# Kernel tuning notes

Measured on AMD Instinct MI355X. Metric: run time of the kernel, lower is better.

The kernel has to match this reference:

```python
import jax, jax.numpy as jnp
import numpy as np

B, C_IN, IMG, PATCH = 16, 3, 512, 16
C_FEAT, N_CLS, K = 2048, 18, 24  # K cells per image (fixed -> jit-friendly ragged groups)
HF = IMG // PATCH  # 32
N_CELLS = B * K
EPS = 1e-6


def setup_inputs() -> dict:
    key = jax.random.key(0)
    ks = jax.random.split(key, 8)
    return {
        "cell_img": jax.random.normal(ks[0], (B, C_IN, IMG, IMG), jnp.float32),
        "cell_masks": jax.random.uniform(ks[1], (N_CELLS, HF, HF), jnp.float32),
        "cell_counts": jnp.full((B,), K, dtype=jnp.int32),
        "W_backbone": jax.random.normal(ks[2], (C_FEAT, C_IN, PATCH, PATCH), jnp.float32) * 0.02,
        "b_backbone": jnp.zeros((C_FEAT,), jnp.float32),
        "W_final": jax.random.normal(ks[3], (N_CLS, C_FEAT, 1, 1), jnp.float32) * 0.02,
        "b_final": jnp.zeros((N_CLS,), jnp.float32),
        "W1": jax.random.normal(ks[4], (1024, C_FEAT), jnp.float32) * 0.02,
        "b1": jnp.zeros((1024,), jnp.float32),
        "W2": jax.random.normal(ks[5], (N_CLS, 1024), jnp.float32) * 0.02,
        "b2": jnp.zeros((N_CLS,), jnp.float32),
    }


def _forward(cell_img, cell_masks, cell_counts, W_backbone, b_backbone,
             W_final, b_final, W1, b1, W2, b2):
    # backbone: patch-embed style conv, 3 -> 2048, stride 16 -> [B, 2048, 32, 32]
    fm = jax.lax.conv_general_dilated(
        cell_img, W_backbone, (PATCH, PATCH), "VALID",
        dimension_numbers=("NCHW", "OIHW", "NCHW"))
    fm = jax.nn.relu(fm + b_backbone[None, :, None, None])
    # final_conv: 1x1 conv 2048 -> 18 class maps
    class_maps = jnp.einsum("bchw,oc->bohw", fm, W_final[:, :, 0, 0]) + b_final[None, :, None, None]

    # masked-RoI average pooling (feature_roi / class_roi)
    fm2 = fm.reshape(B, C_FEAT, HF * HF)            # [B, C, P]
    cm2 = class_maps.reshape(B, N_CLS, HF * HF)     # [B, 18, P]
    masksB = cell_masks.reshape(B, K, HF * HF)      # [B, K, P]
    area = masksB.sum(-1, keepdims=True) + EPS       # [B, K, 1]
    cell_features = jnp.einsum("bkp,bcp->bkc", masksB, fm2) / area   # [B, K, 2048]
    cell_class_logits = jnp.einsum("bkp,bcp->bkc", masksB, cm2) / area  # [B, K, 18]

    # fc_cell_weights (Dropout is identity at eval)
    h = jax.nn.relu(jnp.einsum("bkc,oc->bko", cell_features, W1) + b1)
    cell_weight_logits = jnp.einsum("bkh,oh->bko", h, W2) + b2       # [B, K, 18]

    # per-image (segment) softmax over cells + attention-weighted sum
    attn = jax.nn.softmax(cell_weight_logits, axis=1)
    logits = (attn * cell_class_logits).sum(axis=1)                  # [B, 18]

    # zero-count fallback: global max-pool of class maps
    fallback = class_maps.max(axis=(2, 3))
    return jnp.where((cell_counts > 0)[:, None], logits, fallback)


def reference(cell_img, cell_masks, cell_counts, W_backbone, b_backbone,
              W_final, b_final, W1, b1, W2, b2):
    return _forward(cell_img, cell_masks, cell_counts, W_backbone, b_backbone,
                    W_final, b_final, W1, b1, W2, b2)
```

## Files before the change

### kernel.cpp

```cpp
#include <hip/hip_runtime.h>
#include <hip/hip_bf16.h>

#define B_      16
#define C_IN    3
#define IMG     512
#define PATCH   16
#define C_FEAT  2048
#define N_CLS   18
#define KCELL   24
#define HF      32
#define P_      (HF*HF)
#define KDIM    (C_IN*PATCH*PATCH)
#define M_GEMM1 (B_*P_)
#define EPS_    1e-6f

typedef __attribute__((ext_vector_type(8))) short bf16x8;
typedef __attribute__((ext_vector_type(4))) float f32x4;
typedef __attribute__((ext_vector_type(4))) unsigned short us4;
typedef __attribute__((ext_vector_type(8))) unsigned short us8;
typedef __attribute__((ext_vector_type(4))) float fl4;

#define DEVFN static __device__ __forceinline__

DEVFN unsigned short f2bf(float f) {
  union { float f; unsigned u; } x; x.f = f;
  unsigned r = (x.u + 0x7fffu + ((x.u >> 16) & 1u)) >> 16;
  return (unsigned short)r;
}
DEVFN unsigned short f2bf_h(float f) {
  __hip_bfloat16 h = __float2bfloat16(f);
  return *reinterpret_cast<unsigned short*>(&h);
}
DEVFN float bf2f(unsigned short u) {
  union { unsigned u; float f; } x; x.u = ((unsigned)u) << 16;
  return x.f;
}
DEVFN f32x4 mfma16(bf16x8 a, bf16x8 b, f32x4 c) {
  return __builtin_amdgcn_mfma_f32_16x16x32_bf16(a, b, c, 0, 0, 0);
}
#define GLOAD16(gp, lp) __builtin_amdgcn_global_load_lds( \
    (const __attribute__((address_space(1))) unsigned int*)(gp), \
    (__attribute__((address_space(3))) unsigned int*)(lp), 16, 0, 0)

#define OFF_A     0u
#define OFF_WB    25165824u
#define OFF_W1    28311552u
#define OFF_W2    32505856u
#define OFF_FM    32542720u
#define OFF_MB    99651584u
#define OFF_AREA  100700160u
#define OFF_CF    100702208u
#define OFF_CL    102275072u
#define OFF_H     102302720u
#define WS_NEED   103089152u

__global__ __launch_bounds__(256) void k_prep(const float* __restrict__ masks,
                                              const float* __restrict__ Wb,
                                              const float* __restrict__ W1,
                                              const float* __restrict__ W2,
                                              unsigned short* __restrict__ mb,
                                              float* __restrict__ area,
                                              unsigned short* __restrict__ Wbb,
                                              unsigned short* __restrict__ W1b,
                                              unsigned short* __restrict__ W2b) {
  int blk = blockIdx.x;
  int t = threadIdx.x;
  if (blk < 512) {
    int b = blk >> 5, m = blk & 31;
    unsigned short* dst = mb + ((size_t)(b * 32 + m)) * P_;
    float s = 0.f;
    if (m < KCELL) {
      const float* src = masks + ((size_t)(b * KCELL + m)) * P_;
      for (int p = t; p < P_; p += 256) { float v = src[p]; s += v; dst[p] = f2bf(v); }
    } else {
      for (int p = t; p < P_; p += 256) dst[p] = 0;
    }
    for (int off = 32; off; off >>= 1) s += __shfl_down(s, off);
    __shared__ float red[4];
    if ((t & 63) == 0) red[t >> 6] = s;
    __syncthreads();
    if (t == 0) area[b * 32 + m] = red[0] + red[1] + red[2] + red[3] + EPS_;
    return;
  }
  const float* src; unsigned short* dst; int local, n;
  if (blk < 1280)      { src = Wb; dst = Wbb; local = blk - 512;  n = C_FEAT * KDIM; }
  else if (blk < 2304) { src = W1; dst = W1b; local = blk - 1280; n = 1024 * C_FEAT; }
  else                 { src = W2; dst = W2b; local = blk - 2304; n = N_CLS * 1024; }
  int i = (local * 256 + t) * 8;
  if (i + 8 <= n) {
    fl4 v0 = *(const fl4*)(src + i);
    fl4 v1 = *(const fl4*)(src + i + 4);
    us8 o;
    o[0] = f2bf(v0[0]); o[1] = f2bf(v0[1]); o[2] = f2bf(v0[2]); o[3] = f2bf(v0[3]);
    o[4] = f2bf(v1[0]); o[5] = f2bf(v1[1]); o[6] = f2bf(v1[2]); o[7] = f2bf(v1[3]);
    *(us8*)(dst + i) = o;
  }
}

__global__ __launch_bounds__(256) void k_gemm1f(const float* __restrict__ img,
                                                const unsigned short* __restrict__ BT,
                                                const float* __restrict__ bias,
                                                unsigned short* __restrict__ CT) {
  __shared__ float          As[8 * 1024];
  __shared__ unsigned short Bs[4 * 2048];
  int bid = blockIdx.x;
  int swz = (bid & 7) * 256 + (bid >> 3);
  int bm = swz >> 4, bn = swz & 15;
  int m0 = bm * 128, n0 = bn * 128;
  int t = threadIdx.x;
  int w = t >> 6, l = t & 63, lr = l & 15, lg = l >> 4;
  int wr = w >> 1, wc = w & 1;

  int arow = t >> 1;
  int am = m0 + arow;
  int ab = am >> 10, ap = am & 1023, ahf = ap >> 5, awf = ap & 31;
  const float* imb = img + ((size_t)(ab * 3) * 512 + (size_t)ahf * 16) * 512 + awf * 16;
  int kq = (t & 1) * 4;

  f32x4 acc[4][4] = {};
  for (int k0 = 0; k0 < KDIM; k0 += 64) {
#pragma unroll
    for (int j = 0; j < 8; ++j) {
      int k = k0 + j * 8 + kq;
      int c = k >> 8, py = (k >> 4) & 15, px = k & 15;
      GLOAD16(imb + ((size_t)c * 512 + py) * 512 + px, As + j * 1024 + t * 4);
    }
#pragma unroll
    for (int g = 0; g < 4; ++g)
      GLOAD16(BT + (size_t)(n0 + (t >> 1)) * KDIM + k0 + g * 16 + (t & 1) * 8,
              Bs + g * 2048 + t * 8);
    __syncthreads();
#pragma unroll
    for (int kk = 0; kk < 64; kk += 32) {
      bf16x8 a[4], bb[4];
#pragma unroll
      for (int mi = 0; mi < 4; ++mi) {
        int row = wr * 64 + mi * 16 + lr;
        int o = (kk >> 3) + lg;
        const float* ap_ = As + o * 1024 + row * 8;
        fl4 lo = *(const fl4*)ap_;
        fl4 hi = *(const fl4*)(ap_ + 4);
        us8 af;
        af[0] = f2bf_h(lo[0]); af[1] = f2bf_h(lo[1]); af[2] = f2bf_h(lo[2]); af[3] = f2bf_h(lo[3]);
        af[4] = f2bf_h(hi[0]); af[5] = f2bf_h(hi[1]); af[6] = f2bf_h(hi[2]); af[7] = f2bf_h(hi[3]);
        a[mi] = *(bf16x8*)&af;
      }
#pragma unroll
      for (int ni = 0; ni < 4; ++ni) {
        int row = wc * 64 + ni * 16 + lr;
        int g = (kk >> 4) + (lg >> 1), half = lg & 1;
        bb[ni] = *(const bf16x8*)(Bs + g * 2048 + row * 16 + half * 8);
      }
#pragma unroll
      for (int mi = 0; mi < 4; ++mi)
#pragma unroll
        for (int ni = 0; ni < 4; ++ni)
          acc[mi][ni] = mfma16(a[mi], bb[ni], acc[mi][ni]);
    }
    __syncthreads();
  }
  int b = m0 >> 10;
  int pbase0 = (m0 & 1023) + wr * 64 + lg * 4;
#pragma unroll
  for (int ni = 0; ni < 4; ++ni) {
    int gcol = n0 + wc * 64 + ni * 16 + lr;
    float bv = bias[gcol];
    unsigned short* crow = CT + ((size_t)(b * C_FEAT + gcol)) * P_;
#pragma unroll
    for (int mi = 0; mi < 4; ++mi) {
      us4 o;
#pragma unroll
      for (int r = 0; r < 4; ++r)
        o[r] = f2bf(fmaxf(acc[mi][ni][r] + bv, 0.f));
      *(us4*)(crow + pbase0 + mi * 16) = o;
    }
  }
}

__global__ __launch_bounds__(256) void k_pool(const unsigned short* __restrict__ mb,
                                              const unsigned short* __restrict__ fmT,
                                              const float* __restrict__ area,
                                              unsigned short* __restrict__ CF) {
  int b = blockIdx.x, ct = blockIdx.y;
  int t = threadIdx.x, w = t >> 6, l = t & 63, lr = l & 15, lg = l >> 4;
  int c0 = ct * 128 + w * 32;
  const unsigned short* mbb = mb + (size_t)b * 32 * P_;
  const unsigned short* fb = fmT + (size_t)b * C_FEAT * P_;
  f32x4 acc[2][2] = {};
#pragma unroll 2
  for (int k0 = 0; k0 < P_; k0 += 32) {
    int kb = k0 + lg * 8;
    bf16x8 a0 = *(const bf16x8*)(mbb + (size_t)lr * P_ + kb);
    bf16x8 a1 = *(const bf16x8*)(mbb + (size_t)(16 + lr) * P_ + kb);
    bf16x8 b0 = *(const bf16x8*)(fb + (size_t)(c0 + lr) * P_ + kb);
    bf16x8 b1 = *(const bf16x8*)(fb + (size_t)(c0 + 16 + lr) * P_ + kb);
    acc[0][0] = mfma16(a0, b0, acc[0][0]);
    acc[1][0] = mfma16(a1, b0, acc[1][0]);
    acc[0][1] = mfma16(a0, b1, acc[0][1]);
    acc[1][1] = mfma16(a1, b1, acc[1][1]);
  }
#pragma unroll
  for (int mt = 0; mt < 2; ++mt)
#pragma unroll
    for (int r = 0; r < 4; ++r) {
      int m = mt * 16 + lg * 4 + r;
      if (m < KCELL) {
        float inv = 1.f / area[b * 32 + m];
#pragma unroll
        for (int nt = 0; nt < 2; ++nt) {
          int c = c0 + nt * 16 + lr;
          CF[((size_t)(b * KCELL + m)) * C_FEAT + c] = f2bf(acc[mt][nt][r] * inv);
        }
      }
    }
}

__global__ __launch_bounds__(256) void k_class_logits(const unsigned short* __restrict__ CF,
                                                      const float* __restrict__ Wf,
                                                      const float* __restrict__ bfin,
                                                      const float* __restrict__ area,
                                                      float* __restrict__ cl) {
  int cell = blockIdx.x;
  int t = threadIdx.x;
  int c0 = t * 8;
  float cf[8];
  bf16x8 v = *(const bf16x8*)(CF + (size_t)cell * C_FEAT + c0);
#pragma unroll
  for (int j = 0; j < 8; ++j) cf[j] = bf2f((unsigned short)v[j]);
  float acc[N_CLS];
#pragma unroll
  for (int o = 0; o < N_CLS; ++o) {
    fl4 w0 = *(const fl4*)(Wf + (size_t)o * C_FEAT + c0);
    fl4 w1 = *(const fl4*)(Wf + (size_t)o * C_FEAT + c0 + 4);
    acc[o] = cf[0]*w0[0] + cf[1]*w0[1] + cf[2]*w0[2] + cf[3]*w0[3]
           + cf[4]*w1[0] + cf[5]*w1[1] + cf[6]*w1[2] + cf[7]*w1[3];
  }
#pragma unroll
  for (int o = 0; o < N_CLS; ++o)
    for (int off = 32; off; off >>= 1) acc[o] += __shfl_down(acc[o], off);
  __shared__ float red[4][N_CLS];
  if ((t & 63) == 0) {
#pragma unroll
    for (int o = 0; o < N_CLS; ++o) red[t >> 6][o] = acc[o];
  }
  __syncthreads();
  if (t < N_CLS) {
    int b = cell / KCELL, m = cell % KCELL;
    float ar = area[b * 32 + m];
    float coeff = (ar - EPS_) / ar;
    cl[(size_t)cell * N_CLS + t] =
        red[0][t] + red[1][t] + red[2][t] + red[3][t] + bfin[t] * coeff;
  }
}

__global__ __launch_bounds__(256) void k_mlp1(const unsigned short* __restrict__ CF,
                                              const unsigned short* __restrict__ W1b,
                                              const float* __restrict__ b1,
                                              unsigned short* __restrict__ h) {
  int wid = blockIdx.x * 4 + (threadIdx.x >> 6);
  int l = threadIdx.x & 63, lr = l & 15, lg = l >> 4;
  int mt = wid >> 6, nt = wid & 63;
  int m0 = mt * 16, n0 = nt * 16;
  f32x4 acc = {};
  for (int k0 = 0; k0 < C_FEAT; k0 += 32) {
    int kb = k0 + lg * 8;
    bf16x8 a = *(const bf16x8*)(CF + (size_t)(m0 + lr) * C_FEAT + kb);
    bf16x8 b = *(const bf16x8*)(W1b + (size_t)(n0 + lr) * C_FEAT + kb);
    acc = mfma16(a, b, acc);
  }
  int col = n0 + lr;
  float bv = b1[col];
#pragma unroll
  for (int r = 0; r < 4; ++r) {
    int row = m0 + lg * 4 + r;
    h[(size_t)row * 1024 + col] = f2bf(fmaxf(acc[r] + bv, 0.f));
  }
}

__global__ __launch_bounds__(512) void k_mlp2_final(const unsigned short* __restrict__ hbf,
                                                    const unsigned short* __restrict__ W2b,
                                                    const float* __restrict__ b2,
                                                    const float* __restrict__ cl,
                                                    float* __restrict__ out) {
  int b = blockIdx.x;
  int t = threadIdx.x;
  __shared__ float wl[KCELL][N_CLS + 2];
  if (t < KCELL * N_CLS) {
    int k = t / N_CLS, o = t % N_CLS;
    const unsigned short* hr = hbf + (size_t)(b * KCELL + k) * 1024;
    const unsigned short* wr = W2b + (size_t)o * 1024;
    float acc = 0.f;
    for (int c = 0; c < 1024; c += 16) {
      bf16x8 hv0 = *(const bf16x8*)(hr + c);
      bf16x8 hv1 = *(const bf16x8*)(hr + c + 8);
      bf16x8 wv0 = *(const bf16x8*)(wr + c);
      bf16x8 wv1 = *(const bf16x8*)(wr + c + 8);
#pragma unroll
      for (int j = 0; j < 8; ++j)
        acc += bf2f((unsigned short)hv0[j]) * bf2f((unsigned short)wv0[j])
             + bf2f((unsigned short)hv1[j]) * bf2f((unsigned short)wv1[j]);
    }
    wl[k][o] = acc + b2[o];
  }
  __syncthreads();
  if (t < N_CLS) {
    float m = -3.4e38f;
    for (int k = 0; k < KCELL; ++k) m = fmaxf(m, wl[k][t]);
    float s = 0.f, num = 0.f;
    for (int k = 0; k < KCELL; ++k) {
      float e = expf(wl[k][t] - m);
      s += e;
      num += e * cl[(size_t)(b * KCELL + k) * N_CLS + t];
    }
    out[b * N_CLS + t] = num / s;
  }
}

__global__ __launch_bounds__(256) void k_fallback(const int* __restrict__ counts,
                                                  const unsigned short* __restrict__ fmT,
                                                  const float* __restrict__ Wf,
                                                  const float* __restrict__ bfin,
                                                  float* __restrict__ out) {
  int b = blockIdx.x;
  if (counts[b] > 0) return;
  int t = threadIdx.x;
  const unsigned short* fb = fmT + (size_t)b * C_FEAT * P_;
  float lmax[N_CLS];
#pragma unroll
  for (int o = 0; o < N_CLS; ++o) lmax[o] = -3.4e38f;
  for (int p = t; p < P_; p += 256) {
    float acc[N_CLS];
#pragma unroll
    for (int o = 0; o < N_CLS; ++o) acc[o] = bfin[o];
    for (int c = 0; c < C_FEAT; ++c) {
      float f = bf2f(fb[(size_t)c * P_ + p]);
#pragma unroll
      for (int o = 0; o < N_CLS; ++o) acc[o] += f * Wf[(size_t)o * C_FEAT + c];
    }
#pragma unroll
    for (int o = 0; o < N_CLS; ++o) lmax[o] = fmaxf(lmax[o], acc[o]);
  }
#pragma unroll
  for (int o = 0; o < N_CLS; ++o)
    for (int off = 32; off; off >>= 1) lmax[o] = fmaxf(lmax[o], __shfl_down(lmax[o], off));
  __shared__ float red[4][N_CLS];
  if ((t & 63) == 0) {
#pragma unroll
    for (int o = 0; o < N_CLS; ++o) red[t >> 6][o] = lmax[o];
  }
  __syncthreads();
  if (t < N_CLS)
    out[b * N_CLS + t] = fmaxf(fmaxf(red[0][t], red[1][t]), fmaxf(red[2][t], red[3][t]));
}

extern "C" void kernel_launch(void* const* d_in, const int* in_sizes, int n_in,
                              void* d_out, int out_size, void* d_ws, size_t ws_size,
                              hipStream_t stream) {
  const float* img    = (const float*)d_in[0];
  const float* masks  = (const float*)d_in[1];
  const int*   counts = (const int*)d_in[2];
  const float* Wb     = (const float*)d_in[3];
  const float* bb     = (const float*)d_in[4];
  const float* Wf     = (const float*)d_in[5];
  const float* bfin   = (const float*)d_in[6];
  const float* W1     = (const float*)d_in[7];
  const float* b1     = (const float*)d_in[8];
  const float* W2     = (const float*)d_in[9];
  const float* b2     = (const float*)d_in[10];
  float* out = (float*)d_out;

  char* ws = (char*)d_ws;
  unsigned short* Wbb  = (unsigned short*)(ws + OFF_WB);
  unsigned short* W1b  = (unsigned short*)(ws + OFF_W1);
  unsigned short* W2b  = (unsigned short*)(ws + OFF_W2);
  unsigned short* fmT  = (unsigned short*)(ws + OFF_FM);
  unsigned short* mbb  = (unsigned short*)(ws + OFF_MB);
  float*          area = (float*)(ws + OFF_AREA);
  unsigned short* CF   = (unsigned short*)(ws + OFF_CF);
  float*          cl   = (float*)(ws + OFF_CL);
  unsigned short* hb   = (unsigned short*)(ws + OFF_H);

  k_prep<<<2313, 256, 0, stream>>>(masks, Wb, W1, W2, mbb, area, Wbb, W1b, W2b);
  k_gemm1f<<<(M_GEMM1 / 128) * (C_FEAT / 128), 256, 0, stream>>>(img, Wbb, bb, fmT);
  k_pool<<<dim3(B_, C_FEAT / 128), 256, 0, stream>>>(mbb, fmT, area, CF);
  k_class_logits<<<B_ * KCELL, 256, 0, stream>>>(CF, Wf, bfin, area, cl);
  k_mlp1<<<(24 * 64) / 4, 256, 0, stream>>>(CF, W1b, b1, hb);
  k_mlp2_final<<<B_, 512, 0, stream>>>(hb, W2b, b2, cl, out);
  k_fallback<<<B_, 256, 0, stream>>>(counts, fmT, Wf, bfin, out);
}
```

Baseline: 280.7 us.

## Fuse masked RoI pooling into backbone GEMM epilogue, drop feature-map round trip

The backbone GEMM now keeps its 128x128 output tile in LDS and multiplies it right away by the masks for that spatial slice. It writes per-slice fp32 partial cell features, so the full bf16 feature map (~64MB) never goes to global memory. A new post kernel sums the 8 slice partials, computes mask areas and class logits, and replaces the separate prep, pool and class-logit kernels. Image tiles are converted to bf16 once on load into a swizzled LDS layout rather than at every fragment read. W1/W2 are converted in the MLP kernels instead of a prep pass. The fallback now recomputes the backbone directly from the image, which is very slow but runs only when a count is zero.

Result: slower. 334.4 us (+19.1%).

```diff
diff --git a/kernel.cpp b/kernel.cpp
--- a/kernel.cpp
+++ b/kernel.cpp
@@ -42,67 +42,30 @@
     (const __attribute__((address_space(1))) unsigned int*)(gp), \
     (__attribute__((address_space(3))) unsigned int*)(lp), 16, 0, 0)
 
-#define OFF_A     0u
+#define OFF_CFP   0u
 #define OFF_WB    25165824u
-#define OFF_W1    28311552u
-#define OFF_W2    32505856u
-#define OFF_FM    32542720u
-#define OFF_MB    99651584u
-#define OFF_AREA  100700160u
 #define OFF_CF    100702208u
 #define OFF_CL    102275072u
 #define OFF_H     102302720u
-#define WS_NEED   103089152u
-
-__global__ __launch_bounds__(256) void k_prep(const float* __restrict__ masks,
-                                              const float* __restrict__ Wb,
-                                              const float* __restrict__ W1,
-                                              const float* __restrict__ W2,
-                                              unsigned short* __restrict__ mb,
-                                              float* __restrict__ area,
-                                              unsigned short* __restrict__ Wbb,
-                                              unsigned short* __restrict__ W1b,
-                                              unsigned short* __restrict__ W2b) {
-  int blk = blockIdx.x;
-  int t = threadIdx.x;
-  if (blk < 512) {
-    int b = blk >> 5, m = blk & 31;
-    unsigned short* dst = mb + ((size_t)(b * 32 + m)) * P_;
-    float s = 0.f;
-    if (m < KCELL) {
-      const float* src = masks + ((size_t)(b * KCELL + m)) * P_;
-      for (int p = t; p < P_; p += 256) { float v = src[p]; s += v; dst[p] = f2bf(v); }
-    } else {
-      for (int p = t; p < P_; p += 256) dst[p] = 0;
-    }
-    for (int off = 32; off; off >>= 1) s += __shfl_down(s, off);
-    __shared__ float red[4];
-    if ((t & 63) == 0) red[t >> 6] = s;
-    __syncthreads();
-    if (t == 0) area[b * 32 + m] = red[0] + red[1] + red[2] + red[3] + EPS_;
-    return;
-  }
-  const float* src; unsigned short* dst; int local, n;
-  if (blk < 1280)      { src = Wb; dst = Wbb; local = blk - 512;  n = C_FEAT * KDIM; }
-  else if (blk < 2304) { src = W1; dst = W1b; local = blk - 1280; n = 1024 * C_FEAT; }
-  else                 { src = W2; dst = W2b; local = blk - 2304; n = N_CLS * 1024; }
-  int i = (local * 256 + t) * 8;
-  if (i + 8 <= n) {
-    fl4 v0 = *(const fl4*)(src + i);
-    fl4 v1 = *(const fl4*)(src + i + 4);
-    us8 o;
-    o[0] = f2bf(v0[0]); o[1] = f2bf(v0[1]); o[2] = f2bf(v0[2]); o[3] = f2bf(v0[3]);
-    o[4] = f2bf(v1[0]); o[5] = f2bf(v1[1]); o[6] = f2bf(v1[2]); o[7] = f2bf(v1[3]);
-    *(us8*)(dst + i) = o;
-  }
-}
-
-__global__ __launch_bounds__(256) void k_gemm1f(const float* __restrict__ img,
-                                                const unsigned short* __restrict__ BT,
-                                                const float* __restrict__ bias,
-                                                unsigned short* __restrict__ CT) {
-  __shared__ float          As[8 * 1024];
-  __shared__ unsigned short Bs[4 * 2048];
+
+__global__ __launch_bounds__(256) void k_prepW(const float* __restrict__ Wb,
+                                               unsigned short* __restrict__ Wbb) {
+  int i = (blockIdx.x * 256 + threadIdx.x) * 8;
+  fl4 v0 = *(const fl4*)(Wb + i);
+  fl4 v1 = *(const fl4*)(Wb + i + 4);
+  us8 o;
+  o[0] = f2bf(v0[0]); o[1] = f2bf(v0[1]); o[2] = f2bf(v0[2]); o[3] = f2bf(v0[3]);
+  o[4] = f2bf(v1[0]); o[5] = f2bf(v1[1]); o[6] = f2bf(v1[2]); o[7] = f2bf(v1[3]);
+  *(us8*)(Wbb + i) = o;
+}
+
+__global__ __launch_bounds__(256) void k_gemm1fp(const float* __restrict__ img,
+                                                 const unsigned short* __restrict__ BT,
+                                                 const float* __restrict__ bias,
+                                                 const float* __restrict__ masks,
+                                                 float* __restrict__ CFpart) {
+  __shared__ unsigned short smem[16384];
+  unsigned short* Bs = smem + 8192;
   int bid = blockIdx.x;
   int swz = (bid & 7) * 256 + (bid >> 3);
   int bm = swz >> 4, bn = swz & 15;
@@ -116,19 +79,24 @@
   int ab = am >> 10, ap = am & 1023, ahf = ap >> 5, awf = ap & 31;
   const float* imb = img + ((size_t)(ab * 3) * 512 + (size_t)ahf * 16) * 512 + awf * 16;
   int kq = (t & 1) * 4;
+  int awx = (arow & 7) << 4;
+  int arx = (lr & 7) << 4;
 
   f32x4 acc[4][4] = {};
   for (int k0 = 0; k0 < KDIM; k0 += 64) {
+#pragma unroll
+    for (int g = 0; g < 4; ++g)
+      GLOAD16(BT + (size_t)(n0 + (t >> 1)) * KDIM + k0 + g * 16 + (t & 1) * 8,
+              Bs + g * 2048 + t * 8);
 #pragma unroll
     for (int j = 0; j < 8; ++j) {
       int k = k0 + j * 8 + kq;
       int c = k >> 8, py = (k >> 4) & 15, px = k & 15;
-      GLOAD16(imb + ((size_t)c * 512 + py) * 512 + px, As + j * 1024 + t * 4);
-    }
-#pragma unroll
-    for (int g = 0; g < 4; ++g)
-      GLOAD16(BT + (size_t)(n0 + (t >> 1)) * KDIM + k0 + g * 16 + (t & 1) * 8,
-              Bs + g * 2048 + t * 8);
+      fl4 v = *(const fl4*)(imb + ((size_t)c * 512 + py) * 512 + px);
+      us4 o;
+      o[0] = f2bf_h(v[0]); o[1] = f2bf_h(v[1]); o[2] = f2bf_h(v[2]); o[3] = f2bf_h(v[3]);
+      *(us4*)((char*)smem + ((arow * 128 + j * 16 + kq * 2) ^ awx)) = o;
+    }
     __syncthreads();
 #pragma unroll
     for (int kk = 0; kk < 64; kk += 32) {
@@ -136,14 +104,7 @@
 #pragma unroll
       for (int mi = 0; mi < 4; ++mi) {
         int row = wr * 64 + mi * 16 + lr;
-        int o = (kk >> 3) + lg;
-        const float* ap_ = As + o * 1024 + row * 8;
-        fl4 lo = *(const fl4*)ap_;
-        fl4 hi = *(const fl4*)(ap_ + 4);
-        us8 af;
-        af[0] = f2bf_h(lo[0]); af[1] = f2bf_h(lo[1]); af[2] = f2bf_h(lo[2]); af[3] = f2bf_h(lo[3]);
-        af[4] = f2bf_h(hi[0]); af[5] = f2bf_h(hi[1]); af[6] = f2bf_h(hi[2]); af[7] = f2bf_h(hi[3]);
-        a[mi] = *(bf16x8*)&af;
+        a[mi] = *(const bf16x8*)((const char*)smem + ((row * 128 + kk * 2 + lg * 16) ^ arx));
       }
 #pragma unroll
       for (int ni = 0; ni < 4; ++ni) {
@@ -159,102 +120,127 @@
     }
     __syncthreads();
   }
+
   int b = m0 >> 10;
-  int pbase0 = (m0 & 1023) + wr * 64 + lg * 4;
+  int p0 = m0 & 1023;
+  int slice = (m0 >> 7) & 7;
+  int pl0 = wr * 64 + lg * 4;
 #pragma unroll
   for (int ni = 0; ni < 4; ++ni) {
     int gcol = n0 + wc * 64 + ni * 16 + lr;
     float bv = bias[gcol];
-    unsigned short* crow = CT + ((size_t)(b * C_FEAT + gcol)) * P_;
+    int cl_ = wc * 64 + ni * 16 + lr;
+    int cwx = (cl_ & 7) << 4;
 #pragma unroll
     for (int mi = 0; mi < 4; ++mi) {
       us4 o;
 #pragma unroll
       for (int r = 0; r < 4; ++r)
-        o[r] = f2bf(fmaxf(acc[mi][ni][r] + bv, 0.f));
-      *(us4*)(crow + pbase0 + mi * 16) = o;
-    }
-  }
-}
-
-__global__ __launch_bounds__(256) void k_pool(const unsigned short* __restrict__ mb,
-                                              const unsigned short* __restrict__ fmT,
-                                              const float* __restrict__ area,
-                                              unsigned short* __restrict__ CF) {
-  int b = blockIdx.x, ct = blockIdx.y;
-  int t = threadIdx.x, w = t >> 6, l = t & 63, lr = l & 15, lg = l >> 4;
-  int c0 = ct * 128 + w * 32;
-  const unsigned short* mbb = mb + (size_t)b * 32 * P_;
-  const unsigned short* fb = fmT + (size_t)b * C_FEAT * P_;
-  f32x4 acc[2][2] = {};
-#pragma unroll 2
-  for (int k0 = 0; k0 < P_; k0 += 32) {
-    int kb = k0 + lg * 8;
-    bf16x8 a0 = *(const bf16x8*)(mbb + (size_t)lr * P_ + kb);
-    bf16x8 a1 = *(const bf16x8*)(mbb + (size_t)(16 + lr) * P_ + kb);
-    bf16x8 b0 = *(const bf16x8*)(fb + (size_t)(c0 + lr) * P_ + kb);
-    bf16x8 b1 = *(const bf16x8*)(fb + (size_t)(c0 + 16 + lr) * P_ + kb);
-    acc[0][0] = mfma16(a0, b0, acc[0][0]);
-    acc[1][0] = mfma16(a1, b0, acc[1][0]);
-    acc[0][1] = mfma16(a0, b1, acc[0][1]);
-    acc[1][1] = mfma16(a1, b1, acc[1][1]);
+        o[r] = f2bf_h(fmaxf(acc[mi][ni][r] + bv, 0.f));
+      *(us4*)((char*)smem + ((cl_ * 256 + (pl0 + mi * 16) * 2) ^ cwx)) = o;
+    }
+  }
+  __syncthreads();
+
+  f32x4 pacc[2][2] = {};
+#pragma unroll
+  for (int ks = 0; ks < 4; ++ks) {
+    int kb = ks * 32 + lg * 8;
+    bf16x8 amk[2];
+#pragma unroll
+    for (int mt = 0; mt < 2; ++mt) {
+      int mrow = mt * 16 + lr;
+      us8 tmp = {};
+      if (mrow < KCELL) {
+        const float* mp = masks + ((size_t)(b * KCELL + mrow)) * P_ + p0 + kb;
+        fl4 u0 = *(const fl4*)mp;
+        fl4 u1 = *(const fl4*)(mp + 4);
+        tmp[0] = f2bf_h(u0[0]); tmp[1] = f2bf_h(u0[1]); tmp[2] = f2bf_h(u0[2]); tmp[3] = f2bf_h(u0[3]);
+        tmp[4] = f2bf_h(u1[0]); tmp[5] = f2bf_h(u1[1]); tmp[6] = f2bf_h(u1[2]); tmp[7] = f2bf_h(u1[3]);
+      }
+      amk[mt] = *(bf16x8*)&tmp;
+    }
+    bf16x8 bfv[2];
+#pragma unroll
+    for (int ct = 0; ct < 2; ++ct) {
+      int cl2 = w * 32 + ct * 16 + lr;
+      bfv[ct] = *(const bf16x8*)((const char*)smem + ((cl2 * 256 + kb * 2) ^ ((cl2 & 7) << 4)));
+    }
+    pacc[0][0] = mfma16(amk[0], bfv[0], pacc[0][0]);
+    pacc[1][0] = mfma16(amk[1], bfv[0], pacc[1][0]);
+    pacc[0][1] = mfma16(amk[0], bfv[1], pacc[0][1]);
+    pacc[1][1] = mfma16(amk[1], bfv[1], pacc[1][1]);
   }
 #pragma unroll
   for (int mt = 0; mt < 2; ++mt)
 #pragma unroll
-    for (int r = 0; r < 4; ++r) {
-      int m = mt * 16 + lg * 4 + r;
-      if (m < KCELL) {
-        float inv = 1.f / area[b * 32 + m];
-#pragma unroll
-        for (int nt = 0; nt < 2; ++nt) {
-          int c = c0 + nt * 16 + lr;
-          CF[((size_t)(b * KCELL + m)) * C_FEAT + c] = f2bf(acc[mt][nt][r] * inv);
-        }
-      }
-    }
-}
-
-__global__ __launch_bounds__(256) void k_class_logits(const unsigned short* __restrict__ CF,
-                                                      const float* __restrict__ Wf,
-                                                      const float* __restrict__ bfin,
-                                                      const float* __restrict__ area,
-                                                      float* __restrict__ cl) {
+    for (int ct = 0; ct < 2; ++ct) {
+      int cg = n0 + w * 32 + ct * 16 + lr;
+#pragma unroll
+      for (int r = 0; r < 4; ++r) {
+        int m = mt * 16 + lg * 4 + r;
+        if (m < KCELL)
+          CFpart[(((size_t)(b * KCELL + m)) * 8 + slice) * C_FEAT + cg] = pacc[mt][ct][r];
+      }
+    }
+}
+
+__global__ __launch_bounds__(256) void k_post(const float* __restrict__ masks,
+                                              const float* __restrict__ CFpart,
+                                              const float* __restrict__ Wf,
+                                              const float* __restrict__ bfin,
+                                              unsigned short* __restrict__ CF,
+                                              float* __restrict__ cl) {
   int cell = blockIdx.x;
   int t = threadIdx.x;
+  fl4 mv = *(const fl4*)(masks + (size_t)cell * P_ + t * 4);
+  float s = mv[0] + mv[1] + mv[2] + mv[3];
+  for (int off = 32; off; off >>= 1) s += __shfl_down(s, off);
+  __shared__ float redA[4];
+  __shared__ float red2[4][N_CLS];
+  if ((t & 63) == 0) redA[t >> 6] = s;
+  __syncthreads();
+  float asum = redA[0] + redA[1] + redA[2] + redA[3];
+  float ar = asum + EPS_;
+  float inv = 1.f / ar;
+  float coeff = asum / ar;
   int c0 = t * 8;
-  float cf[8];
-  bf16x8 v = *(const bf16x8*)(CF + (size_t)cell * C_FEAT + c0);
-#pragma unroll
-  for (int j = 0; j < 8; ++j) cf[j] = bf2f((unsigned short)v[j]);
+  float cf[8] = {};
+#pragma unroll
+  for (int s8 = 0; s8 < 8; ++s8) {
+    const float* base = CFpart + ((size_t)cell * 8 + s8) * C_FEAT + c0;
+    fl4 a = *(const fl4*)base;
+    fl4 b = *(const fl4*)(base + 4);
+    cf[0] += a[0]; cf[1] += a[1]; cf[2] += a[2]; cf[3] += a[3];
+    cf[4] += b[0]; cf[5] += b[1]; cf[6] += b[2]; cf[7] += b[3];
+  }
+  us8 o;
+#pragma unroll
+  for (int j = 0; j < 8; ++j) { cf[j] *= inv; o[j] = f2bf(cf[j]); }
+  *(us8*)(CF + (size_t)cell * C_FEAT + c0) = o;
   float acc[N_CLS];
 #pragma unroll
-  for (int o = 0; o < N_CLS; ++o) {
-    fl4 w0 = *(const fl4*)(Wf + (size_t)o * C_FEAT + c0);
-    fl4 w1 = *(const fl4*)(Wf + (size_t)o * C_FEAT + c0 + 4);
-    acc[o] = cf[0]*w0[0] + cf[1]*w0[1] + cf[2]*w0[2] + cf[3]*w0[3]
-           + cf[4]*w1[0] + cf[5]*w1[1] + cf[6]*w1[2] + cf[7]*w1[3];
-  }
-#pragma unroll
-  for (int o = 0; o < N_CLS; ++o)
-    for (int off = 32; off; off >>= 1) acc[o] += __shfl_down(acc[o], off);
-  __shared__ float red[4][N_CLS];
+  for (int oo = 0; oo < N_CLS; ++oo) {
+    fl4 w0 = *(const fl4*)(Wf + (size_t)oo * C_FEAT + c0);
+    fl4 w1 = *(const fl4*)(Wf + (size_t)oo * C_FEAT + c0 + 4);
+    acc[oo] = cf[0]*w0[0] + cf[1]*w0[1] + cf[2]*w0[2] + cf[3]*w0[3]
+            + cf[4]*w1[0] + cf[5]*w1[1] + cf[6]*w1[2] + cf[7]*w1[3];
+  }
+#pragma unroll
+  for (int oo = 0; oo < N_CLS; ++oo)
+    for (int off = 32; off; off >>= 1) acc[oo] += __shfl_down(acc[oo], off);
   if ((t & 63) == 0) {
 #pragma unroll
-    for (int o = 0; o < N_CLS; ++o) red[t >> 6][o] = acc[o];
-  }
-  __syncthreads();
-  if (t < N_CLS) {
-    int b = cell / KCELL, m = cell % KCELL;
-    float ar = area[b * 32 + m];
-    float coeff = (ar - EPS_) / ar;
+    for (int oo = 0; oo < N_CLS; ++oo) red2[t >> 6][oo] = acc[oo];
+  }
+  __syncthreads();
+  if (t < N_CLS)
     cl[(size_t)cell * N_CLS + t] =
-        red[0][t] + red[1][t] + red[2][t] + red[3][t] + bfin[t] * coeff;
-  }
+        red2[0][t] + red2[1][t] + red2[2][t] + red2[3][t] + bfin[t] * coeff;
 }
 
 __global__ __launch_bounds__(256) void k_mlp1(const unsigned short* __restrict__ CF,
-                                              const unsigned short* __restrict__ W1b,
+                                              const float* __restrict__ W1,
                                               const float* __restrict__ b1,
                                               unsigned short* __restrict__ h) {
   int wid = blockIdx.x * 4 + (threadIdx.x >> 6);
@@ -265,8 +251,13 @@
   for (int k0 = 0; k0 < C_FEAT; k0 += 32) {
     int kb = k0 + lg * 8;
     bf16x8 a = *(const bf16x8*)(CF + (size_t)(m0 + lr) * C_FEAT + kb);
-    bf16x8 b = *(const bf16x8*)(W1b + (size_t)(n0 + lr) * C_FEAT + kb);
-    acc = mfma16(a, b, acc);
+    const float* wp = W1 + (size_t)(n0 + lr) * C_FEAT + kb;
+    fl4 w0 = *(const fl4*)wp;
+    fl4 w1 = *(const fl4*)(wp + 4);
+    us8 bw;
+    bw[0] = f2bf_h(w0[0]); bw[1] = f2bf_h(w0[1]); bw[2] = f2bf_h(w0[2]); bw[3] = f2bf_h(w0[3]);
+    bw[4] = f2bf_h(w1[0]); bw[5] = f2bf_h(w1[1]); bw[6] = f2bf_h(w1[2]); bw[7] = f2bf_h(w1[3]);
+    acc = mfma16(a, *(bf16x8*)&bw, acc);
   }
   int col = n0 + lr;
   float bv = b1[col];
@@ -278,7 +269,7 @@
 }
 
 __global__ __launch_bounds__(512) void k_mlp2_final(const unsigned short* __restrict__ hbf,
-                                                    const unsigned short* __restrict__ W2b,
+                                                    const float* __restrict__ W2,
                                                     const float* __restrict__ b2,
                                                     const float* __restrict__ cl,
                                                     float* __restrict__ out) {
@@ -288,17 +279,16 @@
   if (t < KCELL * N_CLS) {
     int k = t / N_CLS, o = t % N_CLS;
     const unsigned short* hr = hbf + (size_t)(b * KCELL + k) * 1024;
-    const unsigned short* wr = W2b + (size_t)o * 1024;
+    const float* wr = W2 + (size_t)o * 1024;
     float acc = 0.f;
-    for (int c = 0; c < 1024; c += 16) {
-      bf16x8 hv0 = *(const bf16x8*)(hr + c);
-      bf16x8 hv1 = *(const bf16x8*)(hr + c + 8);
-      bf16x8 wv0 = *(const bf16x8*)(wr + c);
-      bf16x8 wv1 = *(const bf16x8*)(wr + c + 8);
-#pragma unroll
-      for (int j = 0; j < 8; ++j)
-        acc += bf2f((unsigned short)hv0[j]) * bf2f((unsigned short)wv0[j])
-             + bf2f((unsigned short)hv1[j]) * bf2f((unsigned short)wv1[j]);
+    for (int c = 0; c < 1024; c += 8) {
+      bf16x8 hv = *(const bf16x8*)(hr + c);
+      fl4 w0 = *(const fl4*)(wr + c);
+      fl4 w1 = *(const fl4*)(wr + c + 4);
+      acc += bf2f((unsigned short)hv[0]) * w0[0] + bf2f((unsigned short)hv[1]) * w0[1]
+           + bf2f((unsigned short)hv[2]) * w0[2] + bf2f((unsigned short)hv[3]) * w0[3]
+           + bf2f((unsigned short)hv[4]) * w1[0] + bf2f((unsigned short)hv[5]) * w1[1]
+           + bf2f((unsigned short)hv[6]) * w1[2] + bf2f((unsigned short)hv[7]) * w1[3];
     }
     wl[k][o] = acc + b2[o];
   }
@@ -317,28 +307,36 @@
 }
 
 __global__ __launch_bounds__(256) void k_fallback(const int* __restrict__ counts,
-                                                  const unsigned short* __restrict__ fmT,
+                                                  const float* __restrict__ img,
+                                                  const float* __restrict__ Wb,
+                                                  const float* __restrict__ bb,
                                                   const float* __restrict__ Wf,
                                                   const float* __restrict__ bfin,
                                                   float* __restrict__ out) {
   int b = blockIdx.x;
   if (counts[b] > 0) return;
   int t = threadIdx.x;
-  const unsigned short* fb = fmT + (size_t)b * C_FEAT * P_;
   float lmax[N_CLS];
 #pragma unroll
   for (int o = 0; o < N_CLS; ++o) lmax[o] = -3.4e38f;
   for (int p = t; p < P_; p += 256) {
-    float acc[N_CLS];
-#pragma unroll
-    for (int o = 0; o < N_CLS; ++o) acc[o] = bfin[o];
+    int hfp = p >> 5, wfp = p & 31;
+    const float* ib = img + ((size_t)(b * 3) * 512 + (size_t)hfp * 16) * 512 + wfp * 16;
+    float accp[N_CLS];
+#pragma unroll
+    for (int o = 0; o < N_CLS; ++o) accp[o] = bfin[o];
     for (int c = 0; c < C_FEAT; ++c) {
-      float f = bf2f(fb[(size_t)c * P_ + p]);
-#pragma unroll
-      for (int o = 0; o < N_CLS; ++o) acc[o] += f * Wf[(size_t)o * C_FEAT + c];
-    }
-#pragma unroll
-    for (int o = 0; o < N_CLS; ++o) lmax[o] = fmaxf(lmax[o], acc[o]);
+      float f = bb[c];
+      const float* wrow = Wb + (size_t)c * KDIM;
+      for (int k = 0; k < KDIM; ++k) {
+        int ci = k >> 8, py = (k >> 4) & 15, px = k & 15;
+        f += wrow[k] * ib[((size_t)ci * 512 + py) * 512 + px];
+      }
+      f = fmaxf(f, 0.f);
+      for (int o = 0; o < N_CLS; ++o) accp[o] += Wf[(size_t)o * C_FEAT + c] * f;
+    }
+#pragma unroll
+    for (int o = 0; o < N_CLS; ++o) lmax[o] = fmaxf(lmax[o], accp[o]);
   }
 #pragma unroll
   for (int o = 0; o < N_CLS; ++o)
@@ -370,21 +368,16 @@
   float* out = (float*)d_out;
 
   char* ws = (char*)d_ws;
-  unsigned short* Wbb  = (unsigned short*)(ws + OFF_WB);
-  unsigned short* W1b  = (unsigned short*)(ws + OFF_W1);
-  unsigned short* W2b  = (unsigned short*)(ws + OFF_W2);
-  unsigned short* fmT  = (unsigned short*)(ws + OFF_FM);
-  unsigned short* mbb  = (unsigned short*)(ws + OFF_MB);
-  float*          area = (float*)(ws + OFF_AREA);
-  unsigned short* CF   = (unsigned short*)(ws + OFF_CF);
-  float*          cl   = (float*)(ws + OFF_CL);
-  unsigned short* hb   = (unsigned short*)(ws + OFF_H);
-
-  k_prep<<<2313, 256, 0, stream>>>(masks, Wb, W1, W2, mbb, area, Wbb, W1b, W2b);
-  k_gemm1f<<<(M_GEMM1 / 128) * (C_FEAT / 128), 256, 0, stream>>>(img, Wbb, bb, fmT);
-  k_pool<<<dim3(B_, C_FEAT / 128), 256, 0, stream>>>(mbb, fmT, area, CF);
-  k_class_logits<<<B_ * KCELL, 256, 0, stream>>>(CF, Wf, bfin, area, cl);
-  k_mlp1<<<(24 * 64) / 4, 256, 0, stream>>>(CF, W1b, b1, hb);
-  k_mlp2_final<<<B_, 512, 0, stream>>>(hb, W2b, b2, cl, out);
-  k_fallback<<<B_, 256, 0, stream>>>(counts, fmT, Wf, bfin, out);
-}
+  float*          CFpart = (float*)(ws + OFF_CFP);
+  unsigned short* Wbb    = (unsigned short*)(ws + OFF_WB);
+  unsigned short* CF     = (unsigned short*)(ws + OFF_CF);
+  float*          cl     = (float*)(ws + OFF_CL);
+  unsigned short* hb     = (unsigned short*)(ws + OFF_H);
+
+  k_prepW<<<768, 256, 0, stream>>>(Wb, Wbb);
+  k_gemm1fp<<<2048, 256, 0, stream>>>(img, Wbb, bb, masks, CFpart);
+  k_post<<<B_ * KCELL, 256, 0, stream>>>(masks, CFpart, Wf, bfin, CF, cl);
+  k_mlp1<<<(24 * 64) / 4, 256, 0, stream>>>(CF, W1, b1, hb);
+  k_mlp2_final<<<B_, 512, 0, stream>>>(hb, W2, b2, cl, out);
+  k_fallback<<<B_, 256, 0, stream>>>(counts, img, Wb, bb, Wf, bfin, out);
+}
```
